# Performance work log

Hardware: AMD Instinct MI355X
Metric: run time of the kernel (lower is better)

The kernel has to match this reference:

```python
import jax, jax.numpy as jnp
import numpy as np

D_MODEL, N_HEAD, D_HEAD, N_LAYERS, D_FF = 1024, 16, 64, 6, 4096
SEQ_LEN, MEM_LEN, BATCH, CLAMP_LEN = 512, 128, 4, 512
LN_EPS = 1e-5


def layernorm(x, g, b):
    mu = jnp.mean(x, axis=-1, keepdims=True)
    var = jnp.var(x, axis=-1, keepdims=True)
    return (x - mu) * jax.lax.rsqrt(var + LN_EPS) * g + b


def rel_shift(x):
    # x: (qlen, rlen, B, H) -> Transformer-XL relative shift
    q, r, b, n = x.shape
    zp = jnp.zeros((q, 1, b, n), x.dtype)
    xp = jnp.concatenate([zp, x], axis=1).reshape(r + 1, q, b, n)
    return xp[1:].reshape(q, r, b, n)


def pos_embedding(klen):
    # sinusoidal embedding on positions klen-1 .. 0, clamped at CLAMP_LEN
    pos = jnp.arange(klen - 1, -1, -1.0, dtype=jnp.float32)
    pos = jnp.minimum(pos, float(CLAMP_LEN))
    inv_freq = 1.0 / (10000.0 ** (jnp.arange(0.0, D_MODEL, 2.0) / D_MODEL))
    sin_inp = pos[:, None] * inv_freq[None, :]  # (klen, D/2)
    return jnp.concatenate([jnp.sin(sin_inp), jnp.cos(sin_inp)], axis=-1)  # (klen, D)


def setup_inputs() -> dict:
    key = jax.random.key(0)
    ks = jax.random.split(key, 16)
    s = 0.02
    return {
        "inputs": jax.random.normal(ks[0], (SEQ_LEN, BATCH, D_MODEL), jnp.float32),
        "mems": jax.random.normal(ks[1], (N_LAYERS, MEM_LEN, BATCH, D_MODEL), jnp.float32),
        "r_w_bias": jax.random.normal(ks[2], (N_HEAD, D_HEAD), jnp.float32) * s,
        "r_r_bias": jax.random.normal(ks[3], (N_HEAD, D_HEAD), jnp.float32) * s,
        "qkv_w": jax.random.normal(ks[4], (N_LAYERS, 3 * N_HEAD * D_HEAD, D_MODEL), jnp.float32) * s,
        "r_w": jax.random.normal(ks[5], (N_LAYERS, N_HEAD * D_HEAD, D_MODEL), jnp.float32) * s,
        "o_w": jax.random.normal(ks[6], (N_LAYERS, D_MODEL, N_HEAD * D_HEAD), jnp.float32) * s,
        "ln1_g": jnp.ones((N_LAYERS, D_MODEL), jnp.float32),
        "ln1_b": jnp.zeros((N_LAYERS, D_MODEL), jnp.float32),
        "ff_w1": jax.random.normal(ks[7], (N_LAYERS, D_FF, D_MODEL), jnp.float32) * s,
        "ff_b1": jnp.zeros((N_LAYERS, D_FF), jnp.float32),
        "ff_w2": jax.random.normal(ks[8], (N_LAYERS, D_MODEL, D_FF), jnp.float32) * s,
        "ff_b2": jnp.zeros((N_LAYERS, D_MODEL), jnp.float32),
        "ln2_g": jnp.ones((N_LAYERS, D_MODEL), jnp.float32),
        "ln2_b": jnp.zeros((N_LAYERS, D_MODEL), jnp.float32),
        "fin_g": jnp.ones((D_MODEL,), jnp.float32),
        "fin_b": jnp.zeros((D_MODEL,), jnp.float32),
    }


def reference(inputs, mems, r_w_bias, r_r_bias, qkv_w, r_w, o_w,
              ln1_g, ln1_b, ff_w1, ff_b1, ff_w2, ff_b2, ln2_g, ln2_b,
              fin_g, fin_b):
    qlen, bsz, _ = inputs.shape
    mlen = mems.shape[1]
    klen = mlen + qlen
    scale = 1.0 / np.sqrt(D_HEAD)

    pos_emb = pos_embedding(klen)  # (klen, D)
    # causal mask with memory: True = masked
    attn_mask = jnp.triu(jnp.ones((qlen, klen), bool), k=1 + mlen)

    x = inputs  # (T, B, D)
    for l in range(N_LAYERS):
        # ---- relative multi-head attention (pre_lnorm) ----
        cat = jnp.concatenate([mems[l], x], axis=0)           # (klen, B, D)
        h = layernorm(cat, ln1_g[l], ln1_b[l])
        w_heads = jnp.einsum('kbd,ed->kbe', h, qkv_w[l])      # (klen, B, 3HD)
        r_head_k = jnp.einsum('kd,ed->ke', pos_emb, r_w[l])   # (klen, HD)
        hd = N_HEAD * D_HEAD
        q = w_heads[-qlen:, :, :hd].reshape(qlen, bsz, N_HEAD, D_HEAD)
        k = w_heads[:, :, hd:2 * hd].reshape(klen, bsz, N_HEAD, D_HEAD)
        v = w_heads[:, :, 2 * hd:].reshape(klen, bsz, N_HEAD, D_HEAD)
        r_head_k = r_head_k.reshape(klen, N_HEAD, D_HEAD)

        AC = jnp.einsum('ibnd,jbnd->ijbn', q + r_w_bias, k)
        BD = rel_shift(jnp.einsum('ibnd,jnd->ijbn', q + r_r_bias, r_head_k))
        score = (AC + BD) * scale                              # (q, k, B, H)
        score = jnp.where(attn_mask[:, :, None, None], -jnp.inf, score)
        prob = jax.nn.softmax(score, axis=1)
        attn_vec = jnp.einsum('ijbn,jbnd->ibnd', prob, v).reshape(qlen, bsz, hd)
        attn_out = jnp.einsum('ibe,de->ibd', attn_vec, o_w[l])
        x = x + attn_out

        # ---- position-wise FFN (pre_lnorm) ----
        hf = layernorm(x, ln2_g[l], ln2_b[l])
        hf = jax.nn.relu(jnp.einsum('ibd,fd->ibf', hf, ff_w1[l]) + ff_b1[l])
        hf = jnp.einsum('ibf,df->ibd', hf, ff_w2[l]) + ff_b2[l]
        x = x + hf

    return layernorm(x, fin_g, fin_b)
```

## Files before the change

kernel.cpp:

```cpp
#include <hip/hip_runtime.h>
#include <math.h>
#include <stdint.h>

#define DM    1024
#define NH    16
#define DH    64
#define NL    6
#define DFF   4096
#define QLEN  512
#define MLEN  128
#define B_    4
#define KL    640
#define CLAMP 512
#define EPS   1e-5f

typedef _Float16 f16x8 __attribute__((ext_vector_type(8)));
typedef _Float16 f16x4 __attribute__((ext_vector_type(4)));
typedef float    f32x4 __attribute__((ext_vector_type(4)));

__device__ __forceinline__ void gload16(const void* g, void* l) {
  __builtin_amdgcn_global_load_lds(
      (const __attribute__((address_space(1))) void*)g,
      (__attribute__((address_space(3))) void*)l, 16, 0, 0);
}

__device__ __forceinline__ float block_sum(float v, float* sm4) {
#pragma unroll
  for (int o = 32; o > 0; o >>= 1) v += __shfl_down(v, o, 64);
  int lane = threadIdx.x & 63, wid = threadIdx.x >> 6;
  if (lane == 0) sm4[wid] = v;
  __syncthreads();
  float r = sm4[0] + sm4[1] + sm4[2] + sm4[3];
  __syncthreads();
  return r;
}

__global__ __launch_bounds__(256) void pos_emb_kernel(_Float16* __restrict__ pe) {
  int p = blockIdx.x;
  float pos = fminf((float)(KL - 1 - p), (float)CLAMP);
  for (int f = threadIdx.x; f < 512; f += 256) {
    float inv = powf(10000.0f, -(float)f * (1.0f / 512.0f));
    float a = pos * inv;
    pe[(size_t)p * DM + f]       = (_Float16)sinf(a);
    pe[(size_t)p * DM + 512 + f] = (_Float16)cosf(a);
  }
}

__global__ __launch_bounds__(256) void cast_w_kernel(
    const float* __restrict__ s0, const float* __restrict__ s1,
    const float* __restrict__ s2, const float* __restrict__ s3,
    const float* __restrict__ s4, _Float16* __restrict__ dst) {
  size_t i = ((size_t)blockIdx.x * 256 + threadIdx.x) * 4;
  const float* src; size_t off;
  if (i < 3145728)      { src = s0; off = 0; }
  else if (i < 4194304) { src = s1; off = 3145728; }
  else if (i < 5242880) { src = s2; off = 4194304; }
  else if (i < 9437184) { src = s3; off = 5242880; }
  else                  { src = s4; off = 9437184; }
  float4 v = *(const float4*)(src + (i - off));
  f16x4 o = { (_Float16)v.x, (_Float16)v.y, (_Float16)v.z, (_Float16)v.w };
  *(f16x4*)(dst + i) = o;
}

template <int OUTF16>
__global__ __launch_bounds__(256) void ln_kernel(
    const float* __restrict__ src0, const float* __restrict__ src1,
    const float* __restrict__ g, const float* __restrict__ b,
    float* __restrict__ outf, _Float16* __restrict__ outh, int rows0) {
  __shared__ float sm4[4];
  int row = blockIdx.x;
  const float* src = (row < rows0) ? (src0 + (size_t)row * DM)
                                   : (src1 + (size_t)(row - rows0) * DM);
  float4 v = ((const float4*)src)[threadIdx.x];
  float mean = block_sum(v.x + v.y + v.z + v.w, sm4) * (1.0f / DM);
  float dx = v.x - mean, dy = v.y - mean, dz = v.z - mean, dw = v.w - mean;
  float var = block_sum(dx * dx + dy * dy + dz * dz + dw * dw, sm4) * (1.0f / DM);
  float rstd = rsqrtf(var + EPS);
  float4 gg = ((const float4*)g)[threadIdx.x];
  float4 bb = ((const float4*)b)[threadIdx.x];
  float ox = dx * rstd * gg.x + bb.x;
  float oy = dy * rstd * gg.y + bb.y;
  float oz = dz * rstd * gg.z + bb.z;
  float ow = dw * rstd * gg.w + bb.w;
  if (OUTF16) {
    f16x4 o = { (_Float16)ox, (_Float16)oy, (_Float16)oz, (_Float16)ow };
    *(f16x4*)(outh + (size_t)row * DM + threadIdx.x * 4) = o;
  } else {
    float4 o = { ox, oy, oz, ow };
    ((float4*)(outf + (size_t)row * DM))[threadIdx.x] = o;
  }
}

template <int BIAS, int RELU, int RESID, int OUTF16>
__global__ __launch_bounds__(256) void gemm_mfma(
    const _Float16* __restrict__ A, const _Float16* __restrict__ B,
    const float* __restrict__ bias, const float* __restrict__ resid,
    float* __restrict__ Cf, _Float16* __restrict__ Ch,
    int M, int N, int K) {
  __shared__ alignas(16) _Float16 As[128 * 32];
  __shared__ alignas(16) _Float16 Bs[128 * 32];
  const int t = threadIdx.x;
  const int lane = t & 63, wid = t >> 6;
  const int m0 = blockIdx.y * 128, n0 = blockIdx.x * 128;
  const int wm = (wid >> 1) * 64, wn = (wid & 1) * 64;

  const int c0 = wid * 64 + lane, c1 = c0 + 256;
  const _Float16* Ap0 = A + (size_t)(m0 + (c0 >> 2)) * K + (c0 & 3) * 8;
  const _Float16* Ap1 = A + (size_t)(m0 + (c1 >> 2)) * K + (c1 & 3) * 8;
  const _Float16* Bp0 = B + (size_t)(n0 + (c0 >> 2)) * K + (c0 & 3) * 8;
  const _Float16* Bp1 = B + (size_t)(n0 + (c1 >> 2)) * K + (c1 & 3) * 8;
  _Float16* Asw0 = &As[wid * 512];
  _Float16* Asw1 = &As[wid * 512 + 2048];
  _Float16* Bsw0 = &Bs[wid * 512];
  _Float16* Bsw1 = &Bs[wid * 512 + 2048];

  f32x4 acc[4][4] = {};
  for (int k0 = 0; k0 < K; k0 += 32) {
    __syncthreads();
    gload16(Ap0 + k0, Asw0);
    gload16(Ap1 + k0, Asw1);
    gload16(Bp0 + k0, Bsw0);
    gload16(Bp1 + k0, Bsw1);
    __syncthreads();
    f16x8 af[4], bf[4];
#pragma unroll
    for (int f = 0; f < 4; ++f) {
      af[f] = *(const f16x8*)&As[(wm + f * 16 + (lane & 15)) * 32 + (lane >> 4) * 8];
      bf[f] = *(const f16x8*)&Bs[(wn + f * 16 + (lane & 15)) * 32 + (lane >> 4) * 8];
    }
#pragma unroll
    for (int i = 0; i < 4; ++i)
#pragma unroll
      for (int j = 0; j < 4; ++j)
        acc[i][j] = __builtin_amdgcn_mfma_f32_16x16x32_f16(af[i], bf[j], acc[i][j], 0, 0, 0);
  }
#pragma unroll
  for (int i = 0; i < 4; ++i) {
#pragma unroll
    for (int j = 0; j < 4; ++j) {
      const int n = n0 + wn + j * 16 + (lane & 15);
      float bv = 0.0f;
      if (BIAS) bv = bias[n];
#pragma unroll
      for (int r = 0; r < 4; ++r) {
        const int m = m0 + wm + i * 16 + (lane >> 4) * 4 + r;
        float v = acc[i][j][r] + bv;
        if (RELU) v = fmaxf(v, 0.0f);
        if (RESID) v += resid[(size_t)m * N + n];
        if (OUTF16) Ch[(size_t)m * N + n] = (_Float16)v;
        else        Cf[(size_t)m * N + n] = v;
      }
    }
  }
}

__global__ __launch_bounds__(256) void gemm_sk(
    const _Float16* __restrict__ A, const _Float16* __restrict__ B,
    _Float16* __restrict__ pk, int M, int N, int K, int Ks) {
  __shared__ alignas(16) _Float16 As[128 * 32];
  __shared__ alignas(16) _Float16 Bs[128 * 32];
  const int t = threadIdx.x;
  const int lane = t & 63, wid = t >> 6;
  const int m0 = blockIdx.y * 128, n0 = blockIdx.x * 128;
  const int z = blockIdx.z;
  const int kbase = z * Ks;
  const int wm = (wid >> 1) * 64, wn = (wid & 1) * 64;

  const int c0 = wid * 64 + lane, c1 = c0 + 256;
  const _Float16* Ap0 = A + (size_t)(m0 + (c0 >> 2)) * K + kbase + (c0 & 3) * 8;
  const _Float16* Ap1 = A + (size_t)(m0 + (c1 >> 2)) * K + kbase + (c1 & 3) * 8;
  const _Float16* Bp0 = B + (size_t)(n0 + (c0 >> 2)) * K + kbase + (c0 & 3) * 8;
  const _Float16* Bp1 = B + (size_t)(n0 + (c1 >> 2)) * K + kbase + (c1 & 3) * 8;
  _Float16* Asw0 = &As[wid * 512];
  _Float16* Asw1 = &As[wid * 512 + 2048];
  _Float16* Bsw0 = &Bs[wid * 512];
  _Float16* Bsw1 = &Bs[wid * 512 + 2048];

  f32x4 acc[4][4] = {};
  for (int k0 = 0; k0 < Ks; k0 += 32) {
    __syncthreads();
    gload16(Ap0 + k0, Asw0);
    gload16(Ap1 + k0, Asw1);
    gload16(Bp0 + k0, Bsw0);
    gload16(Bp1 + k0, Bsw1);
    __syncthreads();
    f16x8 af[4], bf[4];
#pragma unroll
    for (int f = 0; f < 4; ++f) {
      af[f] = *(const f16x8*)&As[(wm + f * 16 + (lane & 15)) * 32 + (lane >> 4) * 8];
      bf[f] = *(const f16x8*)&Bs[(wn + f * 16 + (lane & 15)) * 32 + (lane >> 4) * 8];
    }
#pragma unroll
    for (int i = 0; i < 4; ++i)
#pragma unroll
      for (int j = 0; j < 4; ++j)
        acc[i][j] = __builtin_amdgcn_mfma_f32_16x16x32_f16(af[i], bf[j], acc[i][j], 0, 0, 0);
  }
  _Float16* out = pk + (size_t)z * M * N;
#pragma unroll
  for (int i = 0; i < 4; ++i)
#pragma unroll
    for (int j = 0; j < 4; ++j) {
      const int n = n0 + wn + j * 16 + (lane & 15);
#pragma unroll
      for (int r = 0; r < 4; ++r) {
        const int m = m0 + wm + i * 16 + (lane >> 4) * 4 + r;
        out[(size_t)m * N + n] = (_Float16)acc[i][j][r];
      }
    }
}

template <int SK, int BIAS, int RELU, int RESID, int OUTF16>
__global__ __launch_bounds__(256) void reduce_k(
    const _Float16* __restrict__ pk, const float* __restrict__ bias,
    const float* __restrict__ resid, float* __restrict__ Cf,
    _Float16* __restrict__ Ch, int MN, int Nmask) {
  const int idx = (blockIdx.x * 256 + threadIdx.x) * 8;
  float s[8] = {};
#pragma unroll
  for (int zz = 0; zz < SK; ++zz) {
    f16x8 v = *(const f16x8*)(pk + (size_t)zz * MN + idx);
#pragma unroll
    for (int e = 0; e < 8; ++e) s[e] += (float)v[e];
  }
  if (BIAS) {
    const int n0 = idx & Nmask;
#pragma unroll
    for (int e = 0; e < 8; ++e) s[e] += bias[n0 + e];
  }
  if (RELU)
#pragma unroll
    for (int e = 0; e < 8; ++e) s[e] = fmaxf(s[e], 0.0f);
  if (RESID) {
    float4 r0 = *(const float4*)(resid + idx);
    float4 r1 = *(const float4*)(resid + idx + 4);
    s[0] += r0.x; s[1] += r0.y; s[2] += r0.z; s[3] += r0.w;
    s[4] += r1.x; s[5] += r1.y; s[6] += r1.z; s[7] += r1.w;
  }
  if (OUTF16) {
    f16x8 o;
#pragma unroll
    for (int e = 0; e < 8; ++e) o[e] = (_Float16)s[e];
    *(f16x8*)(Ch + idx) = o;
  } else {
    float4 o0 = { s[0], s[1], s[2], s[3] };
    float4 o1 = { s[4], s[5], s[6], s[7] };
    *(float4*)(Cf + idx) = o0;
    *(float4*)(Cf + idx + 4) = o1;
  }
}

__global__ __launch_bounds__(256) void attn_kernel(
    const _Float16* __restrict__ wh,
    const _Float16* __restrict__ rk,
    const float* __restrict__ rwb,
    const float* __restrict__ rrb,
    _Float16* __restrict__ av) {
  __shared__ alignas(16) char smem[62976];
  _Float16* QW = (_Float16*)smem;
  _Float16* QQ = QW + 64 * 72;
  _Float16* RR = QQ + 64 * 72;
  _Float16* KS = RR + 128 * 72;
  _Float16* QRF = KS + 64 * 72;
  _Float16* PS = QRF;

  const int i0 = blockIdx.x * 64, n = blockIdx.y, b = blockIdx.z;
  const int t = threadIdx.x, lane = t & 63, wid = t >> 6;
  const int g = lane >> 4, li = lane & 15;
  const int strip = wid * 16;

  {
    int row = t >> 2, c = (t & 3) * 16;
    const _Float16* qp = wh + ((size_t)(MLEN + i0 + row) * B_ + b) * 3072 + n * 64 + c;
    f16x8 q0 = *(const f16x8*)qp, q1 = *(const f16x8*)(qp + 8);
    f16x8 a0, a1, b0, b1;
#pragma unroll
    for (int e = 0; e < 8; ++e) {
      float f0 = (float)q0[e], f1 = (float)q1[e];
      a0[e] = (_Float16)(f0 + rwb[n * 64 + c + e]);
      a1[e] = (_Float16)(f1 + rwb[n * 64 + c + 8 + e]);
      b0[e] = (_Float16)(f0 + rrb[n * 64 + c + e]);
      b1[e] = (_Float16)(f1 + rrb[n * 64 + c + 8 + e]);
    }
    *(f16x8*)&QW[row * 72 + c] = a0;
    *(f16x8*)&QW[row * 72 + c + 8] = a1;
    *(f16x8*)&QQ[row * 72 + c] = b0;
    *(f16x8*)&QQ[row * 72 + c + 8] = b1;
  }

  f32x4 o_[4] = {};
  float mrun[4], lrun[4];
#pragma unroll
  for (int r = 0; r < 4; ++r) { mrun[r] = -INFINITY; lrun[r] = 0.0f; }

  const int jend = i0 + 192;
  for (int j0 = 0; j0 < jend; j0 += 64) {
    __syncthreads();
    {
      int row = t >> 2, c = (t & 3) * 16;
      const _Float16* kp = wh + ((size_t)(j0 + row) * B_ + b) * 3072 + 1024 + n * 64 + c;
      *(f16x8*)&KS[row * 72 + c] = *(const f16x8*)kp;
      *(f16x8*)&KS[row * 72 + c + 8] = *(const f16x8*)(kp + 8);
    }
    {
      int row = t >> 1, c = (t & 1) * 32;
      int mrow = j0 - i0 + 448 + row;
      if (mrow > KL - 1) mrow = KL - 1;
      const _Float16* rp = rk + (size_t)mrow * DM + n * 64 + c;
#pragma unroll
      for (int cc = 0; cc < 32; cc += 8)
        *(f16x8*)&RR[row * 72 + c + cc] = *(const f16x8*)(rp + cc);
    }
    __syncthreads();
    f32x4 acs[4] = {};
    f32x4 acq[8] = {};
#pragma unroll
    for (int ks_ = 0; ks_ < 2; ++ks_) {
      f16x8 aw = *(const f16x8*)&QW[(strip + li) * 72 + ks_ * 32 + g * 8];
      f16x8 ar = *(const f16x8*)&QQ[(strip + li) * 72 + ks_ * 32 + g * 8];
#pragma unroll
      for (int cf = 0; cf < 4; ++cf) {
        f16x8 bk = *(const f16x8*)&KS[(cf * 16 + li) * 72 + ks_ * 32 + g * 8];
        acs[cf] = __builtin_amdgcn_mfma_f32_16x16x32_f16(aw, bk, acs[cf], 0, 0, 0);
      }
#pragma unroll
      for (int cf = 0; cf < 8; ++cf) {
        f16x8 br = *(const f16x8*)&RR[(cf * 16 + li) * 72 + ks_ * 32 + g * 8];
        acq[cf] = __builtin_amdgcn_mfma_f32_16x16x32_f16(ar, br, acq[cf], 0, 0, 0);
      }
    }
#pragma unroll
    for (int cf = 0; cf < 8; ++cf)
#pragma unroll
      for (int r = 0; r < 4; ++r)
        QRF[(strip + g * 4 + r) * 132 + cf * 16 + li] = (_Float16)acq[cf][r];
    __syncthreads();
    float pf[4][4], fac[4];
#pragma unroll
    for (int r = 0; r < 4; ++r) {
      int il = strip + g * 4 + r, gi = i0 + il;
      float sv[4], mx = -INFINITY;
#pragma unroll
      for (int cf = 0; cf < 4; ++cf) {
        int jl = cf * 16 + li;
        int m = jl - il + 63;
        float v = (acs[cf][r] + (float)QRF[il * 132 + m]) * 0.125f;
        if (j0 + jl > gi + MLEN) v = -INFINITY;
        sv[cf] = v;
        mx = fmaxf(mx, v);
      }
#pragma unroll
      for (int o2 = 1; o2 < 16; o2 <<= 1) mx = fmaxf(mx, __shfl_xor(mx, o2, 64));
      float mnew = fmaxf(mrun[r], mx);
      float fc = expf(mrun[r] - mnew);
      float sum = 0.0f;
#pragma unroll
      for (int cf = 0; cf < 4; ++cf) { pf[cf][r] = expf(sv[cf] - mnew); sum += pf[cf][r]; }
#pragma unroll
      for (int o2 = 1; o2 < 16; o2 <<= 1) sum += __shfl_xor(sum, o2, 64);
      lrun[r] = lrun[r] * fc + sum;
      mrun[r] = mnew;
      fac[r] = fc;
    }
    __syncthreads();
#pragma unroll
    for (int cf = 0; cf < 4; ++cf)
#pragma unroll
      for (int r = 0; r < 4; ++r)
        PS[(strip + g * 4 + r) * 72 + cf * 16 + li] = (_Float16)pf[cf][r];
#pragma unroll
    for (int it = 0; it < 2; ++it) {
      int j = t & 63, d0 = (t >> 6) * 8 + it * 32;
      f16x8 vv = *(const f16x8*)(wh + ((size_t)(j0 + j) * B_ + b) * 3072 + 2048 + n * 64 + d0);
#pragma unroll
      for (int e = 0; e < 8; ++e) KS[(d0 + e) * 72 + j] = vv[e];
    }
    __syncthreads();
#pragma unroll
    for (int cf = 0; cf < 4; ++cf)
#pragma unroll
      for (int r = 0; r < 4; ++r)
        o_[cf][r] *= fac[r];
#pragma unroll
    for (int ks_ = 0; ks_ < 2; ++ks_) {
      f16x8 pa = *(const f16x8*)&PS[(strip + li) * 72 + ks_ * 32 + g * 8];
#pragma unroll
      for (int cf = 0; cf < 4; ++cf) {
        f16x8 bv = *(const f16x8*)&KS[(cf * 16 + li) * 72 + ks_ * 32 + g * 8];
        o_[cf] = __builtin_amdgcn_mfma_f32_16x16x32_f16(pa, bv, o_[cf], 0, 0, 0);
      }
    }
  }
#pragma unroll
  for (int cf = 0; cf < 4; ++cf)
#pragma unroll
    for (int r = 0; r < 4; ++r) {
      int row = strip + g * 4 + r;
      av[((size_t)(i0 + row) * B_ + b) * 1024 + n * 64 + cf * 16 + li] =
          (_Float16)(o_[cf][r] / lrun[r]);
    }
}

extern "C" void kernel_launch(void* const* d_in, const int* in_sizes, int n_in,
                              void* d_out, int out_size, void* d_ws, size_t ws_size,
                              hipStream_t stream) {
  const float* inputs = (const float*)d_in[0];
  const float* mems   = (const float*)d_in[1];
  const float* rwb    = (const float*)d_in[2];
  const float* rrb    = (const float*)d_in[3];
  const float* qkv_w  = (const float*)d_in[4];
  const float* r_w    = (const float*)d_in[5];
  const float* o_w    = (const float*)d_in[6];
  const float* ln1_g  = (const float*)d_in[7];
  const float* ln1_b  = (const float*)d_in[8];
  const float* ff_w1  = (const float*)d_in[9];
  const float* ff_b1  = (const float*)d_in[10];
  const float* ff_w2  = (const float*)d_in[11];
  const float* ff_b2  = (const float*)d_in[12];
  const float* ln2_g  = (const float*)d_in[13];
  const float* ln2_b  = (const float*)d_in[14];
  const float* fin_g  = (const float*)d_in[15];
  const float* fin_b  = (const float*)d_in[16];
  float* out = (float*)d_out;

  float* ws = (float*)d_ws;
  float* xbuf = ws;
  _Float16* fb = (_Float16*)(ws + 2097152);
  _Float16* wh_h  = fb;
  _Float16* rk_h  = wh_h + 7864320;
  _Float16* pe_h  = rk_h + 655360;
  _Float16* h_h   = pe_h + 655360;
  _Float16* av_h  = h_h + 2621440;
  _Float16* ffh_h = av_h + 2097152;
  _Float16* wb_h  = ffh_h + 8388608;
  _Float16* wq = wb_h;
  _Float16* wr = wb_h + 3145728;
  _Float16* wo = wb_h + 4194304;
  _Float16* w1 = wb_h + 5242880;
  _Float16* w2 = wb_h + 9437184;
  _Float16* pk_big = wh_h;
  _Float16* pk_rk  = ffh_h;

  pos_emb_kernel<<<KL, 256, 0, stream>>>(pe_h);

  const float* xcur = inputs;
  for (int l = 0; l < NL; ++l) {
    cast_w_kernel<<<13312, 256, 0, stream>>>(
        qkv_w + (size_t)l * 3145728, r_w + (size_t)l * 1048576,
        o_w + (size_t)l * 1048576, ff_w1 + (size_t)l * 4194304,
        ff_w2 + (size_t)l * 4194304, wb_h);
    ln_kernel<1><<<KL * B_, 256, 0, stream>>>(
        mems + (size_t)l * MLEN * B_ * DM, xcur,
        ln1_g + l * DM, ln1_b + l * DM, nullptr, h_h, MLEN * B_);
    gemm_mfma<0, 0, 0, 1><<<dim3(3072 / 128, 2560 / 128), 256, 0, stream>>>(
        h_h, wq, nullptr, nullptr, nullptr, wh_h, 2560, 3072, DM);
    gemm_sk<<<dim3(DM / 128, KL / 128, 8), 256, 0, stream>>>(
        pe_h, wr, pk_rk, KL, DM, DM, DM / 8);
    reduce_k<8, 0, 0, 0, 1><<<KL * DM / 2048, 256, 0, stream>>>(
        pk_rk, nullptr, nullptr, nullptr, rk_h, KL * DM, DM - 1);
    attn_kernel<<<dim3(QLEN / 64, NH, B_), 256, 0, stream>>>(wh_h, rk_h, rwb, rrb, av_h);
    gemm_sk<<<dim3(DM / 128, (QLEN * B_) / 128, 4), 256, 0, stream>>>(
        av_h, wo, pk_big, QLEN * B_, DM, DM, DM / 4);
    reduce_k<4, 0, 0, 1, 0><<<QLEN * B_ * DM / 2048, 256, 0, stream>>>(
        pk_big, nullptr, xcur, xbuf, nullptr, QLEN * B_ * DM, DM - 1);
    ln_kernel<1><<<QLEN * B_, 256, 0, stream>>>(
        xbuf, nullptr, ln2_g + l * DM, ln2_b + l * DM, nullptr, h_h, 1 << 30);
    gemm_mfma<1, 1, 0, 1><<<dim3(DFF / 128, (QLEN * B_) / 128), 256, 0, stream>>>(
        h_h, w1, ff_b1 + (size_t)l * DFF, nullptr, nullptr, ffh_h, QLEN * B_, DFF, DM);
    gemm_sk<<<dim3(DM / 128, (QLEN * B_) / 128, 4), 256, 0, stream>>>(
        ffh_h, w2, pk_big, QLEN * B_, DM, DFF, DFF / 4);
    reduce_k<4, 1, 0, 1, 0><<<QLEN * B_ * DM / 2048, 256, 0, stream>>>(
        pk_big, ff_b2 + (size_t)l * DM, xbuf, xbuf, nullptr, QLEN * B_ * DM, DM - 1);
    xcur = xbuf;
  }
  ln_kernel<0><<<QLEN * B_, 256, 0, stream>>>(xbuf, nullptr, fin_g, fin_b, out, nullptr, 1 << 30);
}
```

Before: 1.235 ms.

## Split attention KV tiles across two blocks and combine partial softmax results

The attention kernel now splits the key-tile loop between two blocks per query tile, interleaving tiles by parity. Each block writes a partial normalized output plus its running max and sum, and a new combine kernel merges the two halves. Q operands are held in registers instead of LDS, the BD scratch is reduced to the 64 shifted columns actually used, and the softmax uses exp2 with a folded log2e scale. This doubles the grid to raise occupancy and cut per-block serial work, at the cost of an extra launch and extra global traffic for the partials.

```diff
diff --git a/kernel.cpp b/kernel.cpp
--- a/kernel.cpp
+++ b/kernel.cpp
@@ -250,42 +250,36 @@
   }
 }
 
-__global__ __launch_bounds__(256) void attn_kernel(
+__global__ __launch_bounds__(256, 4) void attn_kernel(
     const _Float16* __restrict__ wh,
     const _Float16* __restrict__ rk,
     const float* __restrict__ rwb,
     const float* __restrict__ rrb,
-    _Float16* __restrict__ av) {
-  __shared__ alignas(16) char smem[62976];
-  _Float16* QW = (_Float16*)smem;
-  _Float16* QQ = QW + 64 * 72;
-  _Float16* RR = QQ + 64 * 72;
-  _Float16* KS = RR + 128 * 72;
-  _Float16* QRF = KS + 64 * 72;
-  _Float16* PS = QRF;
-
-  const int i0 = blockIdx.x * 64, n = blockIdx.y, b = blockIdx.z;
+    _Float16* __restrict__ po,
+    float* __restrict__ pm,
+    float* __restrict__ pl) {
+  __shared__ alignas(16) _Float16 RR[128 * 72];
+  __shared__ alignas(16) _Float16 KS[64 * 72];
+  __shared__ alignas(16) _Float16 QS[64 * 72];
+
+  const int i0 = blockIdx.x * 64, n = blockIdx.y;
+  const int b = blockIdx.z & 3, zz = blockIdx.z >> 2;
   const int t = threadIdx.x, lane = t & 63, wid = t >> 6;
   const int g = lane >> 4, li = lane & 15;
   const int strip = wid * 16;
 
-  {
-    int row = t >> 2, c = (t & 3) * 16;
-    const _Float16* qp = wh + ((size_t)(MLEN + i0 + row) * B_ + b) * 3072 + n * 64 + c;
-    f16x8 q0 = *(const f16x8*)qp, q1 = *(const f16x8*)(qp + 8);
-    f16x8 a0, a1, b0, b1;
+  f16x8 qw[2], qr[2];
+#pragma unroll
+  for (int ks_ = 0; ks_ < 2; ++ks_) {
+    const _Float16* qp =
+        wh + ((size_t)(MLEN + i0 + strip + li) * B_ + b) * 3072 + n * 64 + ks_ * 32 + g * 8;
+    f16x8 qv = *(const f16x8*)qp;
 #pragma unroll
     for (int e = 0; e < 8; ++e) {
-      float f0 = (float)q0[e], f1 = (float)q1[e];
-      a0[e] = (_Float16)(f0 + rwb[n * 64 + c + e]);
-      a1[e] = (_Float16)(f1 + rwb[n * 64 + c + 8 + e]);
-      b0[e] = (_Float16)(f0 + rrb[n * 64 + c + e]);
-      b1[e] = (_Float16)(f1 + rrb[n * 64 + c + 8 + e]);
-    }
-    *(f16x8*)&QW[row * 72 + c] = a0;
-    *(f16x8*)&QW[row * 72 + c + 8] = a1;
-    *(f16x8*)&QQ[row * 72 + c] = b0;
-    *(f16x8*)&QQ[row * 72 + c + 8] = b1;
+      float f0 = (float)qv[e];
+      qw[ks_][e] = (_Float16)(f0 + rwb[n * 64 + ks_ * 32 + g * 8 + e]);
+      qr[ks_][e] = (_Float16)(f0 + rrb[n * 64 + ks_ * 32 + g * 8 + e]);
+    }
   }
 
   f32x4 o_[4] = {};
@@ -293,8 +287,10 @@
 #pragma unroll
   for (int r = 0; r < 4; ++r) { mrun[r] = -INFINITY; lrun[r] = 0.0f; }
 
-  const int jend = i0 + 192;
-  for (int j0 = 0; j0 < jend; j0 += 64) {
+  const float SC = 0.125f * 1.44269504f;
+  const int ntiles = i0 / 64 + 3;
+  for (int tt = zz; tt < ntiles; tt += 2) {
+    const int j0 = tt * 64;
     __syncthreads();
     {
       int row = t >> 2, c = (t & 3) * 16;
@@ -313,27 +309,32 @@
     }
     __syncthreads();
     f32x4 acs[4] = {};
-    f32x4 acq[8] = {};
-#pragma unroll
-    for (int ks_ = 0; ks_ < 2; ++ks_) {
-      f16x8 aw = *(const f16x8*)&QW[(strip + li) * 72 + ks_ * 32 + g * 8];
-      f16x8 ar = *(const f16x8*)&QQ[(strip + li) * 72 + ks_ * 32 + g * 8];
+#pragma unroll
+    for (int ks_ = 0; ks_ < 2; ++ks_)
 #pragma unroll
       for (int cf = 0; cf < 4; ++cf) {
         f16x8 bk = *(const f16x8*)&KS[(cf * 16 + li) * 72 + ks_ * 32 + g * 8];
-        acs[cf] = __builtin_amdgcn_mfma_f32_16x16x32_f16(aw, bk, acs[cf], 0, 0, 0);
+        acs[cf] = __builtin_amdgcn_mfma_f32_16x16x32_f16(qw[ks_], bk, acs[cf], 0, 0, 0);
       }
 #pragma unroll
-      for (int cf = 0; cf < 8; ++cf) {
-        f16x8 br = *(const f16x8*)&RR[(cf * 16 + li) * 72 + ks_ * 32 + g * 8];
-        acq[cf] = __builtin_amdgcn_mfma_f32_16x16x32_f16(ar, br, acq[cf], 0, 0, 0);
-      }
-    }
-#pragma unroll
-    for (int cf = 0; cf < 8; ++cf)
-#pragma unroll
-      for (int r = 0; r < 4; ++r)
-        QRF[(strip + g * 4 + r) * 132 + cf * 16 + li] = (_Float16)acq[cf][r];
+    for (int half = 0; half < 2; ++half) {
+      f32x4 acq[4] = {};
+#pragma unroll
+      for (int ks_ = 0; ks_ < 2; ++ks_)
+#pragma unroll
+        for (int cf = 0; cf < 4; ++cf) {
+          f16x8 br = *(const f16x8*)&RR[((half * 4 + cf) * 16 + li) * 72 + ks_ * 32 + g * 8];
+          acq[cf] = __builtin_amdgcn_mfma_f32_16x16x32_f16(qr[ks_], br, acq[cf], 0, 0, 0);
+        }
+#pragma unroll
+      for (int cf = 0; cf < 4; ++cf)
+#pragma unroll
+        for (int r = 0; r < 4; ++r) {
+          int il = strip + g * 4 + r;
+          int jl = (half * 4 + cf) * 16 + li - 63 + il;
+          if ((unsigned)jl < 64u) QS[il * 72 + jl] = (_Float16)acq[cf][r];
+        }
+    }
     __syncthreads();
     float pf[4][4], fac[4];
 #pragma unroll
@@ -343,8 +344,7 @@
 #pragma unroll
       for (int cf = 0; cf < 4; ++cf) {
         int jl = cf * 16 + li;
-        int m = jl - il + 63;
-        float v = (acs[cf][r] + (float)QRF[il * 132 + m]) * 0.125f;
+        float v = (acs[cf][r] + (float)QS[il * 72 + jl]) * SC;
         if (j0 + jl > gi + MLEN) v = -INFINITY;
         sv[cf] = v;
         mx = fmaxf(mx, v);
@@ -352,10 +352,10 @@
 #pragma unroll
       for (int o2 = 1; o2 < 16; o2 <<= 1) mx = fmaxf(mx, __shfl_xor(mx, o2, 64));
       float mnew = fmaxf(mrun[r], mx);
-      float fc = expf(mrun[r] - mnew);
+      float fc = exp2f(mrun[r] - mnew);
       float sum = 0.0f;
 #pragma unroll
-      for (int cf = 0; cf < 4; ++cf) { pf[cf][r] = expf(sv[cf] - mnew); sum += pf[cf][r]; }
+      for (int cf = 0; cf < 4; ++cf) { pf[cf][r] = exp2f(sv[cf] - mnew); sum += pf[cf][r]; }
 #pragma unroll
       for (int o2 = 1; o2 < 16; o2 <<= 1) sum += __shfl_xor(sum, o2, 64);
       lrun[r] = lrun[r] * fc + sum;
@@ -367,7 +367,7 @@
     for (int cf = 0; cf < 4; ++cf)
 #pragma unroll
       for (int r = 0; r < 4; ++r)
-        PS[(strip + g * 4 + r) * 72 + cf * 16 + li] = (_Float16)pf[cf][r];
+        QS[(strip + g * 4 + r) * 72 + cf * 16 + li] = (_Float16)pf[cf][r];
 #pragma unroll
     for (int it = 0; it < 2; ++it) {
       int j = t & 63, d0 = (t >> 6) * 8 + it * 32;
@@ -383,7 +383,7 @@
         o_[cf][r] *= fac[r];
 #pragma unroll
     for (int ks_ = 0; ks_ < 2; ++ks_) {
-      f16x8 pa = *(const f16x8*)&PS[(strip + li) * 72 + ks_ * 32 + g * 8];
+      f16x8 pa = *(const f16x8*)&QS[(strip + li) * 72 + ks_ * 32 + g * 8];
 #pragma unroll
       for (int cf = 0; cf < 4; ++cf) {
         f16x8 bv = *(const f16x8*)&KS[(cf * 16 + li) * 72 + ks_ * 32 + g * 8];
@@ -391,14 +391,44 @@
       }
     }
   }
+  const size_t obase = (size_t)zz * (QLEN * B_ * 1024);
 #pragma unroll
   for (int cf = 0; cf < 4; ++cf)
 #pragma unroll
     for (int r = 0; r < 4; ++r) {
       int row = strip + g * 4 + r;
-      av[((size_t)(i0 + row) * B_ + b) * 1024 + n * 64 + cf * 16 + li] =
-          (_Float16)(o_[cf][r] / lrun[r]);
-    }
+      float l = lrun[r];
+      float oo = (l > 0.0f) ? o_[cf][r] / l : 0.0f;
+      po[obase + ((size_t)(i0 + row) * B_ + b) * 1024 + n * 64 + cf * 16 + li] = (_Float16)oo;
+    }
+  if (li == 0) {
+#pragma unroll
+    for (int r = 0; r < 4; ++r) {
+      int row = strip + g * 4 + r;
+      int idx = ((i0 + row) * B_ + b) * 16 + n;
+      pm[zz * 32768 + idx] = (lrun[r] > 0.0f) ? mrun[r] : -3.0e38f;
+      pl[zz * 32768 + idx] = lrun[r];
+    }
+  }
+}
+
+__global__ __launch_bounds__(256) void attn_combine(
+    const _Float16* __restrict__ po, const float* __restrict__ pm,
+    const float* __restrict__ pl, _Float16* __restrict__ av) {
+  const size_t e = ((size_t)blockIdx.x * 256 + threadIdx.x) * 8;
+  const int mlidx = (int)(e >> 10) * 16 + (((int)e & 1023) >> 6);
+  float m1 = pm[mlidx], m2 = pm[32768 + mlidx];
+  float l1 = pl[mlidx], l2 = pl[32768 + mlidx];
+  float M = fmaxf(m1, m2);
+  float w1 = l1 * exp2f(m1 - M), w2 = l2 * exp2f(m2 - M);
+  float inv = 1.0f / (w1 + w2);
+  w1 *= inv; w2 *= inv;
+  f16x8 o1 = *(const f16x8*)(po + e);
+  f16x8 o2 = *(const f16x8*)(po + 2097152 + e);
+  f16x8 o;
+#pragma unroll
+  for (int k = 0; k < 8; ++k) o[k] = (_Float16)(w1 * (float)o1[k] + w2 * (float)o2[k]);
+  *(f16x8*)(av + e) = o;
 }
 
 extern "C" void kernel_launch(void* const* d_in, const int* in_sizes, int n_in,
@@ -440,6 +470,9 @@
   _Float16* w2 = wb_h + 9437184;
   _Float16* pk_big = wh_h;
   _Float16* pk_rk  = ffh_h;
+  _Float16* po     = ffh_h;
+  float*    pm     = (float*)(ffh_h + 4194304);
+  float*    pl     = pm + 65536;
 
   pos_emb_kernel<<<KL, 256, 0, stream>>>(pe_h);
 
@@ -458,7 +491,9 @@
         pe_h, wr, pk_rk, KL, DM, DM, DM / 8);
     reduce_k<8, 0, 0, 0, 1><<<KL * DM / 2048, 256, 0, stream>>>(
         pk_rk, nullptr, nullptr, nullptr, rk_h, KL * DM, DM - 1);
-    attn_kernel<<<dim3(QLEN / 64, NH, B_), 256, 0, stream>>>(wh_h, rk_h, rwb, rrb, av_h);
+    attn_kernel<<<dim3(QLEN / 64, NH, B_ * 2), 256, 0, stream>>>(
+        wh_h, rk_h, rwb, rrb, po, pm, pl);
+    attn_combine<<<1024, 256, 0, stream>>>(po, pm, pl, av_h);
     gemm_sk<<<dim3(DM / 128, (QLEN * B_) / 128, 4), 256, 0, stream>>>(
         av_h, wo, pk_big, QLEN * B_, DM, DM, DM / 4);
     reduce_k<4, 0, 0, 1, 0><<<QLEN * B_ * DM / 2048, 256, 0, stream>>>(
```

Result: no change. 1.227 ms (-0.7%).
